# Kernel optimization log

Hardware: AMD Instinct MI355X
Metric: run time of the kernel (lower is better)

The kernel has to match this reference:

```python
import jax, jax.numpy as jnp
import numpy as np

N = 50000      # nodes
DEG = 16       # fixed out-degree per row
E = N * DEG    # edges (CSR nnz)
H = 128        # hidden_size
NH = 8         # num_heads


def setup_inputs() -> dict:
    key = jax.random.key(0)
    ks = jax.random.split(key, 8)
    s = 1.0 / np.sqrt(H)
    h = jax.random.normal(ks[0], (N, H), jnp.float32)
    Wq = jax.random.normal(ks[1], (H, H), jnp.float32) * s
    bq = jax.random.normal(ks[2], (H,), jnp.float32) * 0.02
    Wk = jax.random.normal(ks[3], (H, H), jnp.float32) * s
    bk = jax.random.normal(ks[4], (H,), jnp.float32) * 0.02
    Wv = jax.random.normal(ks[5], (H, H), jnp.float32) * s
    bv = jax.random.normal(ks[6], (H,), jnp.float32) * 0.02
    row_ptr = jnp.arange(N + 1, dtype=jnp.int32) * DEG            # fixed-degree CSR
    col_ind = jax.random.randint(ks[7], (E,), 0, N, dtype=jnp.int32)
    return {"h": h, "Wq": Wq, "bq": bq, "Wk": Wk, "bk": bk, "Wv": Wv, "bv": bv,
            "row_ptr": row_ptr, "col_ind": col_ind, "num_heads": NH}


def reference(h, Wq, bq, Wk, bk, Wv, bv, row_ptr, col_ind, num_heads):
    n = h.shape[0]
    hidden = h.shape[1]
    head_dim = hidden // num_heads
    scaling = head_dim ** (-0.5)
    e = col_ind.shape[0]
    # CSR nnz -> row index per edge
    row = (jnp.searchsorted(row_ptr, jnp.arange(e, dtype=row_ptr.dtype), side="right") - 1).astype(jnp.int32)

    # projections; reshape to (N, head_dim, num_heads) exactly as in the torch code
    q = ((h @ Wq.T + bq) * scaling).reshape(n, head_dim, num_heads)
    k = (h @ Wk.T + bk).reshape(n, head_dim, num_heads)
    v = (h @ Wv.T + bv).reshape(n, head_dim, num_heads)

    # bsddmm: per-edge, per-head dot product over head_dim
    scores = jnp.einsum("edh,edh->eh", q[row], k[col_ind])      # [E, NH]

    # sparse row-wise softmax (segment softmax over edges of each row)
    m = jax.ops.segment_max(scores, row, num_segments=n)        # [N, NH]
    ex = jnp.exp(scores - m[row])
    denom = jax.ops.segment_sum(ex, row, num_segments=n)        # [N, NH]
    attn = ex / denom[row]                                      # [E, NH]

    # bspmm: out[i] = sum_{j in nbr(i)} attn[ij] * v[j]
    out = jax.ops.segment_sum(attn[:, None, :] * v[col_ind], row, num_segments=n)  # [N, head_dim, NH]
    return out.reshape(n, -1)
```

## Files before the change

### kernel.cpp

```cpp
#include <hip/hip_runtime.h>
#include <hip/hip_bf16.h>


typedef unsigned short ushort_t;
typedef unsigned int uint32;
typedef short short8 __attribute__((ext_vector_type(8)));
typedef short short4v __attribute__((ext_vector_type(4)));
typedef float f32x4 __attribute__((ext_vector_type(4)));

#define HID 128
#define DEG 16
#define OSTRIDE_LDS 132

__device__ __forceinline__ float bf2f(ushort_t u) {
  uint32 x = ((uint32)u) << 16;
  return __builtin_bit_cast(float, x);
}
__device__ __forceinline__ ushort_t f2bf(float f) {
  uint32 u = __builtin_bit_cast(uint32, f);
  u += 0x7fffu + ((u >> 16) & 1u);
  return (ushort_t)(u >> 16);
}

__device__ __forceinline__ void split2(float x, float y, uint32& hi, uint32& lo) {
  __hip_bfloat162 h2 = __float22bfloat162_rn(float2{x, y});
  __builtin_memcpy(&hi, &h2, 4);
  float hx = __builtin_bit_cast(float, hi << 16);
  float hy = __builtin_bit_cast(float, hi & 0xffff0000u);
  __hip_bfloat162 l2 = __float22bfloat162_rn(float2{x - hx, y - hy});
  __builtin_memcpy(&lo, &l2, 4);
}

__device__ __forceinline__ void split8v(float4 a, float4 b, short8& hi, short8& lo) {
  uint32* hu = (uint32*)&hi;
  uint32* lu = (uint32*)&lo;
  split2(a.x, a.y, hu[0], lu[0]);
  split2(a.z, a.w, hu[1], lu[1]);
  split2(b.x, b.y, hu[2], lu[2]);
  split2(b.z, b.w, hu[3], lu[3]);
}

__device__ __forceinline__ void split8p(const float* __restrict__ p, short8& hi, short8& lo) {
  float4 a = *(const float4*)p;
  float4 b = *(const float4*)(p + 4);
  split8v(a, b, hi, lo);
}

__global__ __launch_bounds__(256) void prep_kernel(
    const float* __restrict__ Wq, const float* __restrict__ Wk,
    const float* __restrict__ Wv,
    ushort_t* __restrict__ whi, ushort_t* __restrict__ wlo) {
  const int idx8 = (blockIdx.x * 256 + threadIdx.x) * 8;
  const float* W = (idx8 < 16384) ? Wq : (idx8 < 32768) ? Wk : Wv;
  const int off = idx8 & 16383;
  short8 hi, lo;
  split8p(W + off, hi, lo);
  *(short8*)(whi + idx8) = hi;
  *(short8*)(wlo + idx8) = lo;
}

__global__ __launch_bounds__(256) void qkv_fused_kernel(
    const float* __restrict__ h,
    const float* __restrict__ bq, const float* __restrict__ bk,
    const float* __restrict__ bv,
    const ushort_t* __restrict__ whi, const ushort_t* __restrict__ wlo,
    ushort_t* __restrict__ qs, ushort_t* __restrict__ ks, ushort_t* __restrict__ vs,
    int n) {
  __shared__ __align__(16) char lds_b[32 * 1024];
  __shared__ ushort_t lds_r[4][32 * OSTRIDE_LDS];

  const int wave = threadIdx.x >> 6;
  const int l = threadIdx.x & 63;
  const int lm = l & 15;
  const int lq = l >> 4;
  const int m0 = blockIdx.x * 128 + wave * 32;

  int ar0 = m0 + lm;        if (ar0 >= n) ar0 = n - 1;
  int ar1 = m0 + 16 + lm;   if (ar1 >= n) ar1 = n - 1;
  const float* ap0 = h + (size_t)ar0 * HID + lq * 8;
  const float* ap1 = h + (size_t)ar1 * HID + lq * 8;
  short8 ah0[4], al0[4], ah1[4], al1[4];
#pragma unroll
  for (int kt = 0; kt < 4; kt++) {
    split8p(ap0 + kt * 32, ah0[kt], al0[kt]);
    split8p(ap1 + kt * 32, ah1[kt], al1[kt]);
  }

#pragma unroll 1
  for (int p = 0; p < 3; p++) {
    const ushort_t* __restrict__ Wh = whi + p * 16384;
    const ushort_t* __restrict__ Wl = wlo + p * 16384;
    const float* __restrict__ bias = (p == 0) ? bq : (p == 1) ? bk : bv;
    ushort_t* __restrict__ outp = (p == 0) ? qs : (p == 1) ? ks : vs;
    const int ostride = (p == 0) ? 256 : 128;
    const float scale = (p == 0) ? 0.25f : 1.0f;

    f32x4 acc[2][8];
#pragma unroll
    for (int f = 0; f < 2; f++)
#pragma unroll
      for (int t = 0; t < 8; t++) acc[f][t] = (f32x4){0.f, 0.f, 0.f, 0.f};

#pragma unroll
    for (int jj = 0; jj < 8; jj++) {
      const int j = wave * 8 + jj, t = j >> 2, kt = j & 3;
      const ushort_t* gp = Wh + (t * 16 + lm) * HID + kt * 32 + lq * 8;
      __builtin_amdgcn_global_load_lds(
          (const __attribute__((address_space(1))) void*)gp,
          (__attribute__((address_space(3))) void*)(lds_b + j * 1024 + l * 16),
          16, 0, 0);
    }
    __syncthreads();
#pragma unroll
    for (int kt = 0; kt < 4; kt++) {
#pragma unroll
      for (int t = 0; t < 8; t++) {
        short8 bh = *(const short8*)(lds_b + (t * 4 + kt) * 1024 + l * 16);
        acc[0][t] = __builtin_amdgcn_mfma_f32_16x16x32_bf16(ah0[kt], bh, acc[0][t], 0, 0, 0);
        acc[0][t] = __builtin_amdgcn_mfma_f32_16x16x32_bf16(al0[kt], bh, acc[0][t], 0, 0, 0);
        acc[1][t] = __builtin_amdgcn_mfma_f32_16x16x32_bf16(ah1[kt], bh, acc[1][t], 0, 0, 0);
        acc[1][t] = __builtin_amdgcn_mfma_f32_16x16x32_bf16(al1[kt], bh, acc[1][t], 0, 0, 0);
      }
    }
    __syncthreads();

#pragma unroll
    for (int jj = 0; jj < 8; jj++) {
      const int j = wave * 8 + jj, t = j >> 2, kt = j & 3;
      const ushort_t* gp = Wl + (t * 16 + lm) * HID + kt * 32 + lq * 8;
      __builtin_amdgcn_global_load_lds(
          (const __attribute__((address_space(1))) void*)gp,
          (__attribute__((address_space(3))) void*)(lds_b + j * 1024 + l * 16),
          16, 0, 0);
    }
    __syncthreads();
#pragma unroll
    for (int kt = 0; kt < 4; kt++) {
#pragma unroll
      for (int t = 0; t < 8; t++) {
        short8 bl = *(const short8*)(lds_b + (t * 4 + kt) * 1024 + l * 16);
        acc[0][t] = __builtin_amdgcn_mfma_f32_16x16x32_bf16(ah0[kt], bl, acc[0][t], 0, 0, 0);
        acc[1][t] = __builtin_amdgcn_mfma_f32_16x16x32_bf16(ah1[kt], bl, acc[1][t], 0, 0, 0);
      }
    }
    __syncthreads();

    ushort_t* lo_ = lds_r[wave];
#pragma unroll
    for (int t = 0; t < 8; t++) {
      const int col = t * 16 + lm;
      const float bv_ = bias[col];
#pragma unroll
      for (int f = 0; f < 2; f++) {
#pragma unroll
        for (int r = 0; r < 4; r++) {
          lo_[(f * 16 + lq * 4 + r) * OSTRIDE_LDS + col] = f2bf((acc[f][t][r] + bv_) * scale);
        }
      }
    }
    asm volatile("s_waitcnt lgkmcnt(0)" ::: "memory");
    __builtin_amdgcn_wave_barrier();

    const int rr = l >> 5;
    const int ch = l & 31;
#pragma unroll
    for (int it = 0; it < 16; it++) {
      const int rw = it * 2 + rr;
      const int grow = m0 + rw;
      short4v val = *(short4v*)(lo_ + rw * OSTRIDE_LDS + ch * 4);
      if (grow < n) *(short4v*)(outp + (size_t)grow * ostride + ch * 4) = val;
    }
  }
}

__global__ __launch_bounds__(256) void attn_kernel(
    const int* __restrict__ col_ind,
    const ushort_t* __restrict__ qs, const ushort_t* __restrict__ ks,
    const ushort_t* __restrict__ vs, float* __restrict__ out, int n) {
  __shared__ __align__(16) float lds_attn[4 * DEG * 8];

  const int wv = threadIdx.x >> 6;
  const int l = threadIdx.x & 63;
  const int lm = l & 15;
  const int lq = l >> 4;

  int row = blockIdx.x * 4 + wv;
  if (row >= n) row = n - 1;
  const int eb = row * DEG;

  const int cm = col_ind[eb + lm];
  const ushort_t* kp = ks + (size_t)cm * HID + lq * 8;
  const ushort_t* qp = qs + (size_t)row * 256;

  short8 af[4];
  ushort_t qv[4];
#pragma unroll
  for (int kt = 0; kt < 4; kt++) {
    af[kt] = *(const short8*)(kp + kt * 32);
    qv[kt] = (lm < 8) ? qp[kt * 32 + lq * 8 + lm] : (ushort_t)0;
  }

  uint32 vreg[DEG];
#pragma unroll
  for (int e = 0; e < DEG; e++) {
    const int c = col_ind[eb + e];
    vreg[e] = *(const uint32*)(vs + (size_t)c * HID + 2 * l);
  }

  f32x4 acc = (f32x4){0.f, 0.f, 0.f, 0.f};
#pragma unroll
  for (int kt = 0; kt < 4; kt++) {
    short8 bf;
#pragma unroll
    for (int j = 0; j < 8; j++) bf[j] = (lm == j) ? (short)qv[kt] : (short)0;
    acc = __builtin_amdgcn_mfma_f32_16x16x32_bf16(af[kt], bf, acc, 0, 0, 0);
  }

  float m = fmaxf(fmaxf(acc[0], acc[1]), fmaxf(acc[2], acc[3]));
  m = fmaxf(m, __shfl_xor(m, 16, 64));
  m = fmaxf(m, __shfl_xor(m, 32, 64));
  float e0 = __expf(acc[0] - m), e1 = __expf(acc[1] - m);
  float e2 = __expf(acc[2] - m), e3 = __expf(acc[3] - m);
  float s = e0 + e1 + e2 + e3;
  s += __shfl_xor(s, 16, 64);
  s += __shfl_xor(s, 32, 64);
  const float inv = 1.0f / s;

  float* ap = &lds_attn[wv * (DEG * 8)];
  if (lm < 8) {
    ap[(lq * 4 + 0) * 8 + lm] = e0 * inv;
    ap[(lq * 4 + 1) * 8 + lm] = e1 * inv;
    ap[(lq * 4 + 2) * 8 + lm] = e2 * inv;
    ap[(lq * 4 + 3) * 8 + lm] = e3 * inv;
  }
  asm volatile("s_waitcnt lgkmcnt(0)" ::: "memory");
  __builtin_amdgcn_wave_barrier();

  const int h0 = 2 * (l & 3);
  float o0 = 0.f, o1 = 0.f;
#pragma unroll
  for (int e = 0; e < DEG; e++) {
    const float2 at = *(const float2*)(ap + e * 8 + h0);
    o0 += at.x * bf2f((ushort_t)(vreg[e] & 0xffffu));
    o1 += at.y * bf2f((ushort_t)(vreg[e] >> 16));
  }

  float2 o = {o0, o1};
  *(float2*)(out + (size_t)row * HID + 2 * l) = o;
}

extern "C" void kernel_launch(void* const* d_in, const int* in_sizes, int n_in,
                              void* d_out, int out_size, void* d_ws, size_t ws_size,
                              hipStream_t stream) {
  const float* h  = (const float*)d_in[0];
  const float* Wq = (const float*)d_in[1];
  const float* bq = (const float*)d_in[2];
  const float* Wk = (const float*)d_in[3];
  const float* bk = (const float*)d_in[4];
  const float* Wv = (const float*)d_in[5];
  const float* bv = (const float*)d_in[6];
  const int* col_ind = (const int*)d_in[8];

  const int n = in_sizes[0] / HID;

  ushort_t* ks  = (ushort_t*)d_ws;
  ushort_t* vs  = ks + (size_t)n * HID;
  ushort_t* whi = vs + (size_t)n * HID;
  ushort_t* wlo = whi + 3 * 16384;
  ushort_t* qs  = (ushort_t*)d_out;
  float* outf   = (float*)d_out;

  prep_kernel<<<24, 256, 0, stream>>>(Wq, Wk, Wv, whi, wlo);
  qkv_fused_kernel<<<(n + 127) / 128, 256, 0, stream>>>(h, bq, bk, bv, whi, wlo, qs, ks, vs, n);
  attn_kernel<<<(n + 3) / 4, 256, 0, stream>>>(col_ind, qs, ks, vs, outf, n);
}
```

Measured before the change: 173.3 us.

## Double-buffer QKV weight staging and process two rows per wave in attention

The QKV projection kernel now uses two LDS weight buffers. It prefetches the next hi/lo weight slab with global_load_lds and waits on a partial vmcnt instead of fully serialising each load before its MFMA pass. The attention kernel now handles two CSR rows per wave, issuing twice as many independent K/V gathers to raise memory-level parallelism. The cost is more LDS in the projection kernel, which may reduce blocks per CU, and higher register pressure in the attention kernel.

```diff
diff --git a/kernel.cpp b/kernel.cpp
--- a/kernel.cpp
+++ b/kernel.cpp
@@ -59,6 +59,91 @@
   *(short8*)(wlo + idx8) = lo;
 }
 
+#define WAITV(n) asm volatile("s_waitcnt vmcnt(" #n ")" ::: "memory")
+#define BARRIER() __builtin_amdgcn_s_barrier()
+#define MEMPIN() asm volatile("" ::: "memory")
+
+__device__ __forceinline__ void stage_w(const ushort_t* __restrict__ W,
+                                        char* lb, int wave, int l) {
+  const int lm = l & 15, lq = l >> 4;
+#pragma unroll
+  for (int jj = 0; jj < 8; jj++) {
+    const int j = wave * 8 + jj, t = j >> 2, kt = j & 3;
+    const ushort_t* gp = W + (t * 16 + lm) * HID + kt * 32 + lq * 8;
+    __builtin_amdgcn_global_load_lds(
+        (const __attribute__((address_space(1))) void*)gp,
+        (__attribute__((address_space(3))) void*)(lb + j * 1024 + l * 16),
+        16, 0, 0);
+  }
+}
+
+__device__ __forceinline__ void mfma_hi(const char* lb, int l,
+    const short8 ah0[4], const short8 al0[4],
+    const short8 ah1[4], const short8 al1[4], f32x4 acc[2][8]) {
+#pragma unroll
+  for (int kt = 0; kt < 4; kt++) {
+#pragma unroll
+    for (int t = 0; t < 8; t++) {
+      short8 bh = *(const short8*)(lb + (t * 4 + kt) * 1024 + l * 16);
+      acc[0][t] = __builtin_amdgcn_mfma_f32_16x16x32_bf16(ah0[kt], bh, acc[0][t], 0, 0, 0);
+      acc[0][t] = __builtin_amdgcn_mfma_f32_16x16x32_bf16(al0[kt], bh, acc[0][t], 0, 0, 0);
+      acc[1][t] = __builtin_amdgcn_mfma_f32_16x16x32_bf16(ah1[kt], bh, acc[1][t], 0, 0, 0);
+      acc[1][t] = __builtin_amdgcn_mfma_f32_16x16x32_bf16(al1[kt], bh, acc[1][t], 0, 0, 0);
+    }
+  }
+}
+
+__device__ __forceinline__ void mfma_lo(const char* lb, int l,
+    const short8 ah0[4], const short8 ah1[4], f32x4 acc[2][8]) {
+#pragma unroll
+  for (int kt = 0; kt < 4; kt++) {
+#pragma unroll
+    for (int t = 0; t < 8; t++) {
+      short8 bl = *(const short8*)(lb + (t * 4 + kt) * 1024 + l * 16);
+      acc[0][t] = __builtin_amdgcn_mfma_f32_16x16x32_bf16(ah0[kt], bl, acc[0][t], 0, 0, 0);
+      acc[1][t] = __builtin_amdgcn_mfma_f32_16x16x32_bf16(ah1[kt], bl, acc[1][t], 0, 0, 0);
+    }
+  }
+}
+
+__device__ __forceinline__ void zero_acc(f32x4 acc[2][8]) {
+#pragma unroll
+  for (int f = 0; f < 2; f++)
+#pragma unroll
+    for (int t = 0; t < 8; t++) acc[f][t] = (f32x4){0.f, 0.f, 0.f, 0.f};
+}
+
+__device__ __forceinline__ void epilogue(f32x4 acc[2][8],
+    const float* __restrict__ bias, ushort_t* __restrict__ outp,
+    int ostride, float scale, ushort_t* lo_, int m0, int n, int l) {
+  const int lm = l & 15, lq = l >> 4;
+#pragma unroll
+  for (int t = 0; t < 8; t++) {
+    const int col = t * 16 + lm;
+    const float bv_ = bias[col];
+#pragma unroll
+    for (int f = 0; f < 2; f++) {
+#pragma unroll
+      for (int r = 0; r < 4; r++) {
+        lo_[(f * 16 + lq * 4 + r) * OSTRIDE_LDS + col] = f2bf((acc[f][t][r] + bv_) * scale);
+      }
+    }
+  }
+  asm volatile("s_waitcnt lgkmcnt(0)" ::: "memory");
+  __builtin_amdgcn_wave_barrier();
+
+  const int rr = l >> 5;
+  const int ch = l & 31;
+#pragma unroll
+  for (int it = 0; it < 16; it++) {
+    const int rw = it * 2 + rr;
+    const int grow = m0 + rw;
+    short4v val = *(short4v*)(lo_ + rw * OSTRIDE_LDS + ch * 4);
+    if (grow < n) *(short4v*)(outp + (size_t)grow * ostride + ch * 4) = val;
+  }
+  MEMPIN();
+}
+
 __global__ __launch_bounds__(256) void qkv_fused_kernel(
     const float* __restrict__ h,
     const float* __restrict__ bq, const float* __restrict__ bk,
@@ -66,7 +151,7 @@
     const ushort_t* __restrict__ whi, const ushort_t* __restrict__ wlo,
     ushort_t* __restrict__ qs, ushort_t* __restrict__ ks, ushort_t* __restrict__ vs,
     int n) {
-  __shared__ __align__(16) char lds_b[32 * 1024];
+  __shared__ __align__(16) char lds_b[2][32 * 1024];
   __shared__ ushort_t lds_r[4][32 * OSTRIDE_LDS];
 
   const int wave = threadIdx.x >> 6;
@@ -75,6 +160,8 @@
   const int lq = l >> 4;
   const int m0 = blockIdx.x * 128 + wave * 32;
 
+  stage_w(whi, lds_b[0], wave, l);
+
   int ar0 = m0 + lm;        if (ar0 >= n) ar0 = n - 1;
   int ar1 = m0 + 16 + lm;   if (ar1 >= n) ar1 = n - 1;
   const float* ap0 = h + (size_t)ar0 * HID + lq * 8;
@@ -86,167 +173,146 @@
     split8p(ap1 + kt * 32, ah1[kt], al1[kt]);
   }
 
-#pragma unroll 1
-  for (int p = 0; p < 3; p++) {
-    const ushort_t* __restrict__ Wh = whi + p * 16384;
-    const ushort_t* __restrict__ Wl = wlo + p * 16384;
-    const float* __restrict__ bias = (p == 0) ? bq : (p == 1) ? bk : bv;
-    ushort_t* __restrict__ outp = (p == 0) ? qs : (p == 1) ? ks : vs;
-    const int ostride = (p == 0) ? 256 : 128;
-    const float scale = (p == 0) ? 0.25f : 1.0f;
-
-    f32x4 acc[2][8];
-#pragma unroll
-    for (int f = 0; f < 2; f++)
-#pragma unroll
-      for (int t = 0; t < 8; t++) acc[f][t] = (f32x4){0.f, 0.f, 0.f, 0.f};
-
-#pragma unroll
-    for (int jj = 0; jj < 8; jj++) {
-      const int j = wave * 8 + jj, t = j >> 2, kt = j & 3;
-      const ushort_t* gp = Wh + (t * 16 + lm) * HID + kt * 32 + lq * 8;
-      __builtin_amdgcn_global_load_lds(
-          (const __attribute__((address_space(1))) void*)gp,
-          (__attribute__((address_space(3))) void*)(lds_b + j * 1024 + l * 16),
-          16, 0, 0);
-    }
-    __syncthreads();
-#pragma unroll
-    for (int kt = 0; kt < 4; kt++) {
-#pragma unroll
-      for (int t = 0; t < 8; t++) {
-        short8 bh = *(const short8*)(lds_b + (t * 4 + kt) * 1024 + l * 16);
-        acc[0][t] = __builtin_amdgcn_mfma_f32_16x16x32_bf16(ah0[kt], bh, acc[0][t], 0, 0, 0);
-        acc[0][t] = __builtin_amdgcn_mfma_f32_16x16x32_bf16(al0[kt], bh, acc[0][t], 0, 0, 0);
-        acc[1][t] = __builtin_amdgcn_mfma_f32_16x16x32_bf16(ah1[kt], bh, acc[1][t], 0, 0, 0);
-        acc[1][t] = __builtin_amdgcn_mfma_f32_16x16x32_bf16(al1[kt], bh, acc[1][t], 0, 0, 0);
-      }
-    }
-    __syncthreads();
-
-#pragma unroll
-    for (int jj = 0; jj < 8; jj++) {
-      const int j = wave * 8 + jj, t = j >> 2, kt = j & 3;
-      const ushort_t* gp = Wl + (t * 16 + lm) * HID + kt * 32 + lq * 8;
-      __builtin_amdgcn_global_load_lds(
-          (const __attribute__((address_space(1))) void*)gp,
-          (__attribute__((address_space(3))) void*)(lds_b + j * 1024 + l * 16),
-          16, 0, 0);
-    }
-    __syncthreads();
-#pragma unroll
-    for (int kt = 0; kt < 4; kt++) {
-#pragma unroll
-      for (int t = 0; t < 8; t++) {
-        short8 bl = *(const short8*)(lds_b + (t * 4 + kt) * 1024 + l * 16);
-        acc[0][t] = __builtin_amdgcn_mfma_f32_16x16x32_bf16(ah0[kt], bl, acc[0][t], 0, 0, 0);
-        acc[1][t] = __builtin_amdgcn_mfma_f32_16x16x32_bf16(ah1[kt], bl, acc[1][t], 0, 0, 0);
-      }
-    }
-    __syncthreads();
-
-    ushort_t* lo_ = lds_r[wave];
-#pragma unroll
-    for (int t = 0; t < 8; t++) {
-      const int col = t * 16 + lm;
-      const float bv_ = bias[col];
-#pragma unroll
-      for (int f = 0; f < 2; f++) {
-#pragma unroll
-        for (int r = 0; r < 4; r++) {
-          lo_[(f * 16 + lq * 4 + r) * OSTRIDE_LDS + col] = f2bf((acc[f][t][r] + bv_) * scale);
-        }
-      }
-    }
-    asm volatile("s_waitcnt lgkmcnt(0)" ::: "memory");
-    __builtin_amdgcn_wave_barrier();
-
-    const int rr = l >> 5;
-    const int ch = l & 31;
-#pragma unroll
-    for (int it = 0; it < 16; it++) {
-      const int rw = it * 2 + rr;
-      const int grow = m0 + rw;
-      short4v val = *(short4v*)(lo_ + rw * OSTRIDE_LDS + ch * 4);
-      if (grow < n) *(short4v*)(outp + (size_t)grow * ostride + ch * 4) = val;
-    }
-  }
+  f32x4 acc[2][8];
+  ushort_t* lo_ = lds_r[wave];
+
+  stage_w(wlo, lds_b[1], wave, l);
+  WAITV(8); BARRIER();
+  zero_acc(acc);
+  mfma_hi(lds_b[0], l, ah0, al0, ah1, al1, acc);
+  BARRIER();
+  stage_w(whi + 16384, lds_b[0], wave, l);
+  WAITV(8); BARRIER();
+  mfma_lo(lds_b[1], l, ah0, ah1, acc);
+  epilogue(acc, bq, qs, 256, 0.25f, lo_, m0, n, l);
+  BARRIER();
+  stage_w(wlo + 16384, lds_b[1], wave, l);
+  WAITV(8); BARRIER();
+  zero_acc(acc);
+  mfma_hi(lds_b[0], l, ah0, al0, ah1, al1, acc);
+  BARRIER();
+  stage_w(whi + 32768, lds_b[0], wave, l);
+  WAITV(8); BARRIER();
+  mfma_lo(lds_b[1], l, ah0, ah1, acc);
+  epilogue(acc, bk, ks, 128, 1.0f, lo_, m0, n, l);
+  BARRIER();
+  stage_w(wlo + 32768, lds_b[1], wave, l);
+  WAITV(8); BARRIER();
+  zero_acc(acc);
+  mfma_hi(lds_b[0], l, ah0, al0, ah1, al1, acc);
+  BARRIER();
+  WAITV(0); BARRIER();
+  mfma_lo(lds_b[1], l, ah0, ah1, acc);
+  epilogue(acc, bv, vs, 128, 1.0f, lo_, m0, n, l);
 }
 
 __global__ __launch_bounds__(256) void attn_kernel(
     const int* __restrict__ col_ind,
     const ushort_t* __restrict__ qs, const ushort_t* __restrict__ ks,
     const ushort_t* __restrict__ vs, float* __restrict__ out, int n) {
-  __shared__ __align__(16) float lds_attn[4 * DEG * 8];
+  __shared__ __align__(16) float lds_attn[4][2][DEG * 8];
 
   const int wv = threadIdx.x >> 6;
   const int l = threadIdx.x & 63;
   const int lm = l & 15;
   const int lq = l >> 4;
 
-  int row = blockIdx.x * 4 + wv;
-  if (row >= n) row = n - 1;
-  const int eb = row * DEG;
-
-  const int cm = col_ind[eb + lm];
-  const ushort_t* kp = ks + (size_t)cm * HID + lq * 8;
-  const ushort_t* qp = qs + (size_t)row * 256;
-
-  short8 af[4];
-  ushort_t qv[4];
-#pragma unroll
-  for (int kt = 0; kt < 4; kt++) {
-    af[kt] = *(const short8*)(kp + kt * 32);
-    qv[kt] = (lm < 8) ? qp[kt * 32 + lq * 8 + lm] : (ushort_t)0;
-  }
-
-  uint32 vreg[DEG];
+  int row0 = (blockIdx.x * 4 + wv) * 2;
+  if (row0 >= n) row0 = n - 1;
+  int row1 = row0 + 1;
+  if (row1 >= n) row1 = n - 1;
+  const int eb0 = row0 * DEG, eb1 = row1 * DEG;
+
+  const int cm0 = col_ind[eb0 + lm];
+  const int cm1 = col_ind[eb1 + lm];
+  const ushort_t* kp0 = ks + (size_t)cm0 * HID + lq * 8;
+  const ushort_t* kp1 = ks + (size_t)cm1 * HID + lq * 8;
+  const ushort_t* qp0 = qs + (size_t)row0 * 256;
+  const ushort_t* qp1 = qs + (size_t)row1 * 256;
+
+  short8 af0[4], af1[4];
+  ushort_t qv0[4], qv1[4];
+#pragma unroll
+  for (int kt = 0; kt < 4; kt++) {
+    af0[kt] = *(const short8*)(kp0 + kt * 32);
+    af1[kt] = *(const short8*)(kp1 + kt * 32);
+    qv0[kt] = (lm < 8) ? qp0[kt * 32 + lq * 8 + lm] : (ushort_t)0;
+    qv1[kt] = (lm < 8) ? qp1[kt * 32 + lq * 8 + lm] : (ushort_t)0;
+  }
+
+  uint32 vreg0[DEG], vreg1[DEG];
 #pragma unroll
   for (int e = 0; e < DEG; e++) {
-    const int c = col_ind[eb + e];
-    vreg[e] = *(const uint32*)(vs + (size_t)c * HID + 2 * l);
-  }
-
-  f32x4 acc = (f32x4){0.f, 0.f, 0.f, 0.f};
-#pragma unroll
-  for (int kt = 0; kt < 4; kt++) {
-    short8 bf;
-#pragma unroll
-    for (int j = 0; j < 8; j++) bf[j] = (lm == j) ? (short)qv[kt] : (short)0;
-    acc = __builtin_amdgcn_mfma_f32_16x16x32_bf16(af[kt], bf, acc, 0, 0, 0);
-  }
-
-  float m = fmaxf(fmaxf(acc[0], acc[1]), fmaxf(acc[2], acc[3]));
-  m = fmaxf(m, __shfl_xor(m, 16, 64));
-  m = fmaxf(m, __shfl_xor(m, 32, 64));
-  float e0 = __expf(acc[0] - m), e1 = __expf(acc[1] - m);
-  float e2 = __expf(acc[2] - m), e3 = __expf(acc[3] - m);
-  float s = e0 + e1 + e2 + e3;
-  s += __shfl_xor(s, 16, 64);
-  s += __shfl_xor(s, 32, 64);
-  const float inv = 1.0f / s;
-
-  float* ap = &lds_attn[wv * (DEG * 8)];
+    const int c0 = col_ind[eb0 + e];
+    const int c1 = col_ind[eb1 + e];
+    vreg0[e] = *(const uint32*)(vs + (size_t)c0 * HID + 2 * l);
+    vreg1[e] = *(const uint32*)(vs + (size_t)c1 * HID + 2 * l);
+  }
+
+  f32x4 acc0 = (f32x4){0.f, 0.f, 0.f, 0.f};
+  f32x4 acc1 = (f32x4){0.f, 0.f, 0.f, 0.f};
+#pragma unroll
+  for (int kt = 0; kt < 4; kt++) {
+    short8 bf0, bf1;
+#pragma unroll
+    for (int j = 0; j < 8; j++) {
+      bf0[j] = (lm == j) ? (short)qv0[kt] : (short)0;
+      bf1[j] = (lm == j) ? (short)qv1[kt] : (short)0;
+    }
+    acc0 = __builtin_amdgcn_mfma_f32_16x16x32_bf16(af0[kt], bf0, acc0, 0, 0, 0);
+    acc1 = __builtin_amdgcn_mfma_f32_16x16x32_bf16(af1[kt], bf1, acc1, 0, 0, 0);
+  }
+
+  float m0 = fmaxf(fmaxf(acc0[0], acc0[1]), fmaxf(acc0[2], acc0[3]));
+  m0 = fmaxf(m0, __shfl_xor(m0, 16, 64));
+  m0 = fmaxf(m0, __shfl_xor(m0, 32, 64));
+  float e00 = __expf(acc0[0] - m0), e01 = __expf(acc0[1] - m0);
+  float e02 = __expf(acc0[2] - m0), e03 = __expf(acc0[3] - m0);
+  float s0 = e00 + e01 + e02 + e03;
+  s0 += __shfl_xor(s0, 16, 64);
+  s0 += __shfl_xor(s0, 32, 64);
+  const float inv0 = 1.0f / s0;
+  float m1 = fmaxf(fmaxf(acc1[0], acc1[1]), fmaxf(acc1[2], acc1[3]));
+  m1 = fmaxf(m1, __shfl_xor(m1, 16, 64));
+  m1 = fmaxf(m1, __shfl_xor(m1, 32, 64));
+  float e10 = __expf(acc1[0] - m1), e11 = __expf(acc1[1] - m1);
+  float e12 = __expf(acc1[2] - m1), e13 = __expf(acc1[3] - m1);
+  float s1 = e10 + e11 + e12 + e13;
+  s1 += __shfl_xor(s1, 16, 64);
+  s1 += __shfl_xor(s1, 32, 64);
+  const float inv1 = 1.0f / s1;
+
+  float* ap0 = lds_attn[wv][0];
+  float* ap1 = lds_attn[wv][1];
   if (lm < 8) {
-    ap[(lq * 4 + 0) * 8 + lm] = e0 * inv;
-    ap[(lq * 4 + 1) * 8 + lm] = e1 * inv;
-    ap[(lq * 4 + 2) * 8 + lm] = e2 * inv;
-    ap[(lq * 4 + 3) * 8 + lm] = e3 * inv;
+    ap0[(lq * 4 + 0) * 8 + lm] = e00 * inv0;
+    ap0[(lq * 4 + 1) * 8 + lm] = e01 * inv0;
+    ap0[(lq * 4 + 2) * 8 + lm] = e02 * inv0;
+    ap0[(lq * 4 + 3) * 8 + lm] = e03 * inv0;
+    ap1[(lq * 4 + 0) * 8 + lm] = e10 * inv1;
+    ap1[(lq * 4 + 1) * 8 + lm] = e11 * inv1;
+    ap1[(lq * 4 + 2) * 8 + lm] = e12 * inv1;
+    ap1[(lq * 4 + 3) * 8 + lm] = e13 * inv1;
   }
   asm volatile("s_waitcnt lgkmcnt(0)" ::: "memory");
   __builtin_amdgcn_wave_barrier();
 
   const int h0 = 2 * (l & 3);
-  float o0 = 0.f, o1 = 0.f;
+  float o00 = 0.f, o01 = 0.f, o10 = 0.f, o11 = 0.f;
 #pragma unroll
   for (int e = 0; e < DEG; e++) {
-    const float2 at = *(const float2*)(ap + e * 8 + h0);
-    o0 += at.x * bf2f((ushort_t)(vreg[e] & 0xffffu));
-    o1 += at.y * bf2f((ushort_t)(vreg[e] >> 16));
-  }
-
-  float2 o = {o0, o1};
-  *(float2*)(out + (size_t)row * HID + 2 * l) = o;
+    const float2 a0 = *(const float2*)(ap0 + e * 8 + h0);
+    const float2 a1 = *(const float2*)(ap1 + e * 8 + h0);
+    o00 += a0.x * bf2f((ushort_t)(vreg0[e] & 0xffffu));
+    o01 += a0.y * bf2f((ushort_t)(vreg0[e] >> 16));
+    o10 += a1.x * bf2f((ushort_t)(vreg1[e] & 0xffffu));
+    o11 += a1.y * bf2f((ushort_t)(vreg1[e] >> 16));
+  }
+
+  float2 oa = {o00, o01};
+  float2 ob = {o10, o11};
+  *(float2*)(out + (size_t)row0 * HID + 2 * l) = oa;
+  *(float2*)(out + (size_t)row1 * HID + 2 * l) = ob;
 }
 
 extern "C" void kernel_launch(void* const* d_in, const int* in_sizes, int n_in,
@@ -270,7 +336,8 @@
   ushort_t* qs  = (ushort_t*)d_out;
   float* outf   = (float*)d_out;
 
+  const int npairs = (n + 1) / 2;
   prep_kernel<<<24, 256, 0, stream>>>(Wq, Wk, Wv, whi, wlo);
   qkv_fused_kernel<<<(n + 127) / 128, 256, 0, stream>>>(h, bq, bk, bv, whi, wlo, qs, ks, vs, n);
-  attn_kernel<<<(n + 3) / 4, 256, 0, stream>>>(col_ind, qs, ks, vs, outf, n);
-}
+  attn_kernel<<<(npairs + 3) / 4, 256, 0, stream>>>(col_ind, qs, ks, vs, outf, n);
+}
```

Result: slower. 192.0 us (+10.8%).

## Double-buffer weight staging in QKV kernel to overlap loads with MFMA

Applied to the files above, without the earlier changes.

Splits each 32 KB weight tile load into two 16 KB halves held in a double-buffered LDS region, and fully unrolls the Q/K/V passes into a software pipeline. The next half-tile is issued with global_load_lds while MFMAs consume the current one, with vmcnt waits and barriers replacing the full syncthreads pairs. Input rows are loaded as raw float4 before weight staging, so the bf16 split overlaps the first loads. The cost is fragile hand-placed waitcnt logic and more straight-line code.

```diff
diff --git a/kernel.cpp b/kernel.cpp
--- a/kernel.cpp
+++ b/kernel.cpp
@@ -59,6 +59,94 @@
   *(short8*)(wlo + idx8) = lo;
 }
 
+#define WAITV(n) asm volatile("s_waitcnt vmcnt(" #n ")" ::: "memory")
+#define BARRIER() __builtin_amdgcn_s_barrier()
+#define MEMPIN() asm volatile("" ::: "memory")
+
+__device__ __forceinline__ void stage_half(const ushort_t* __restrict__ W,
+                                           char* lb, int half, int wave, int l) {
+  const int lm = l & 15, lq = l >> 4;
+#pragma unroll
+  for (int jj = 0; jj < 4; jj++) {
+    const int j = half * 16 + wave * 4 + jj;
+    const int t = j >> 2, kt = j & 3;
+    const ushort_t* gp = W + (t * 16 + lm) * HID + kt * 32 + lq * 8;
+    __builtin_amdgcn_global_load_lds(
+        (const __attribute__((address_space(1))) void*)gp,
+        (__attribute__((address_space(3))) void*)(lb + (j & 15) * 1024 + l * 16),
+        16, 0, 0);
+  }
+}
+
+__device__ __forceinline__ void mfma_half_hi(const char* lb, int tbase, int l,
+    const short8 ah0[4], const short8 al0[4],
+    const short8 ah1[4], const short8 al1[4], f32x4 acc[2][8]) {
+#pragma unroll
+  for (int kt = 0; kt < 4; kt++) {
+#pragma unroll
+    for (int tt = 0; tt < 4; tt++) {
+      const int t = tbase + tt;
+      short8 bh = *(const short8*)(lb + (tt * 4 + kt) * 1024 + l * 16);
+      acc[0][t] = __builtin_amdgcn_mfma_f32_16x16x32_bf16(ah0[kt], bh, acc[0][t], 0, 0, 0);
+      acc[0][t] = __builtin_amdgcn_mfma_f32_16x16x32_bf16(al0[kt], bh, acc[0][t], 0, 0, 0);
+      acc[1][t] = __builtin_amdgcn_mfma_f32_16x16x32_bf16(ah1[kt], bh, acc[1][t], 0, 0, 0);
+      acc[1][t] = __builtin_amdgcn_mfma_f32_16x16x32_bf16(al1[kt], bh, acc[1][t], 0, 0, 0);
+    }
+  }
+}
+
+__device__ __forceinline__ void mfma_half_lo(const char* lb, int tbase, int l,
+    const short8 ah0[4], const short8 ah1[4], f32x4 acc[2][8]) {
+#pragma unroll
+  for (int kt = 0; kt < 4; kt++) {
+#pragma unroll
+    for (int tt = 0; tt < 4; tt++) {
+      const int t = tbase + tt;
+      short8 bl = *(const short8*)(lb + (tt * 4 + kt) * 1024 + l * 16);
+      acc[0][t] = __builtin_amdgcn_mfma_f32_16x16x32_bf16(ah0[kt], bl, acc[0][t], 0, 0, 0);
+      acc[1][t] = __builtin_amdgcn_mfma_f32_16x16x32_bf16(ah1[kt], bl, acc[1][t], 0, 0, 0);
+    }
+  }
+}
+
+__device__ __forceinline__ void zero_acc(f32x4 acc[2][8]) {
+#pragma unroll
+  for (int f = 0; f < 2; f++)
+#pragma unroll
+    for (int t = 0; t < 8; t++) acc[f][t] = (f32x4){0.f, 0.f, 0.f, 0.f};
+}
+
+__device__ __forceinline__ void epilogue(f32x4 acc[2][8],
+    const float* __restrict__ bias, ushort_t* __restrict__ outp,
+    int ostride, float scale, ushort_t* lo_, int m0, int n, int l) {
+  const int lm = l & 15, lq = l >> 4;
+#pragma unroll
+  for (int t = 0; t < 8; t++) {
+    const int col = t * 16 + lm;
+    const float bv_ = bias[col];
+#pragma unroll
+    for (int f = 0; f < 2; f++) {
+#pragma unroll
+      for (int r = 0; r < 4; r++) {
+        lo_[(f * 16 + lq * 4 + r) * OSTRIDE_LDS + col] = f2bf((acc[f][t][r] + bv_) * scale);
+      }
+    }
+  }
+  asm volatile("s_waitcnt lgkmcnt(0)" ::: "memory");
+  __builtin_amdgcn_wave_barrier();
+
+  const int rr = l >> 5;
+  const int ch = l & 31;
+#pragma unroll
+  for (int it = 0; it < 16; it++) {
+    const int rw = it * 2 + rr;
+    const int grow = m0 + rw;
+    short4v val = *(short4v*)(lo_ + rw * OSTRIDE_LDS + ch * 4);
+    if (grow < n) *(short4v*)(outp + (size_t)grow * ostride + ch * 4) = val;
+  }
+  MEMPIN();
+}
+
 __global__ __launch_bounds__(256) void qkv_fused_kernel(
     const float* __restrict__ h,
     const float* __restrict__ bq, const float* __restrict__ bk,
@@ -66,7 +154,7 @@
     const ushort_t* __restrict__ whi, const ushort_t* __restrict__ wlo,
     ushort_t* __restrict__ qs, ushort_t* __restrict__ ks, ushort_t* __restrict__ vs,
     int n) {
-  __shared__ __align__(16) char lds_b[32 * 1024];
+  __shared__ __align__(16) char lds_b[2][16 * 1024];
   __shared__ ushort_t lds_r[4][32 * OSTRIDE_LDS];
 
   const int wave = threadIdx.x >> 6;
@@ -79,98 +167,79 @@
   int ar1 = m0 + 16 + lm;   if (ar1 >= n) ar1 = n - 1;
   const float* ap0 = h + (size_t)ar0 * HID + lq * 8;
   const float* ap1 = h + (size_t)ar1 * HID + lq * 8;
+  float4 a0[4][2], a1[4][2];
+#pragma unroll
+  for (int kt = 0; kt < 4; kt++) {
+    a0[kt][0] = *(const float4*)(ap0 + kt * 32);
+    a0[kt][1] = *(const float4*)(ap0 + kt * 32 + 4);
+    a1[kt][0] = *(const float4*)(ap1 + kt * 32);
+    a1[kt][1] = *(const float4*)(ap1 + kt * 32 + 4);
+  }
+
+  stage_half(whi, lds_b[0], 0, wave, l);
+  stage_half(whi, lds_b[1], 1, wave, l);
+
   short8 ah0[4], al0[4], ah1[4], al1[4];
 #pragma unroll
   for (int kt = 0; kt < 4; kt++) {
-    split8p(ap0 + kt * 32, ah0[kt], al0[kt]);
-    split8p(ap1 + kt * 32, ah1[kt], al1[kt]);
-  }
-
-#pragma unroll 1
-  for (int p = 0; p < 3; p++) {
-    const ushort_t* __restrict__ Wh = whi + p * 16384;
-    const ushort_t* __restrict__ Wl = wlo + p * 16384;
-    const float* __restrict__ bias = (p == 0) ? bq : (p == 1) ? bk : bv;
-    ushort_t* __restrict__ outp = (p == 0) ? qs : (p == 1) ? ks : vs;
-    const int ostride = (p == 0) ? 256 : 128;
-    const float scale = (p == 0) ? 0.25f : 1.0f;
-
-    f32x4 acc[2][8];
-#pragma unroll
-    for (int f = 0; f < 2; f++)
-#pragma unroll
-      for (int t = 0; t < 8; t++) acc[f][t] = (f32x4){0.f, 0.f, 0.f, 0.f};
-
-#pragma unroll
-    for (int jj = 0; jj < 8; jj++) {
-      const int j = wave * 8 + jj, t = j >> 2, kt = j & 3;
-      const ushort_t* gp = Wh + (t * 16 + lm) * HID + kt * 32 + lq * 8;
-      __builtin_amdgcn_global_load_lds(
-          (const __attribute__((address_space(1))) void*)gp,
-          (__attribute__((address_space(3))) void*)(lds_b + j * 1024 + l * 16),
-          16, 0, 0);
-    }
-    __syncthreads();
-#pragma unroll
-    for (int kt = 0; kt < 4; kt++) {
-#pragma unroll
-      for (int t = 0; t < 8; t++) {
-        short8 bh = *(const short8*)(lds_b + (t * 4 + kt) * 1024 + l * 16);
-        acc[0][t] = __builtin_amdgcn_mfma_f32_16x16x32_bf16(ah0[kt], bh, acc[0][t], 0, 0, 0);
-        acc[0][t] = __builtin_amdgcn_mfma_f32_16x16x32_bf16(al0[kt], bh, acc[0][t], 0, 0, 0);
-        acc[1][t] = __builtin_amdgcn_mfma_f32_16x16x32_bf16(ah1[kt], bh, acc[1][t], 0, 0, 0);
-        acc[1][t] = __builtin_amdgcn_mfma_f32_16x16x32_bf16(al1[kt], bh, acc[1][t], 0, 0, 0);
-      }
-    }
-    __syncthreads();
-
-#pragma unroll
-    for (int jj = 0; jj < 8; jj++) {
-      const int j = wave * 8 + jj, t = j >> 2, kt = j & 3;
-      const ushort_t* gp = Wl + (t * 16 + lm) * HID + kt * 32 + lq * 8;
-      __builtin_amdgcn_global_load_lds(
-          (const __attribute__((address_space(1))) void*)gp,
-          (__attribute__((address_space(3))) void*)(lds_b + j * 1024 + l * 16),
-          16, 0, 0);
-    }
-    __syncthreads();
-#pragma unroll
-    for (int kt = 0; kt < 4; kt++) {
-#pragma unroll
-      for (int t = 0; t < 8; t++) {
-        short8 bl = *(const short8*)(lds_b + (t * 4 + kt) * 1024 + l * 16);
-        acc[0][t] = __builtin_amdgcn_mfma_f32_16x16x32_bf16(ah0[kt], bl, acc[0][t], 0, 0, 0);
-        acc[1][t] = __builtin_amdgcn_mfma_f32_16x16x32_bf16(ah1[kt], bl, acc[1][t], 0, 0, 0);
-      }
-    }
-    __syncthreads();
-
-    ushort_t* lo_ = lds_r[wave];
-#pragma unroll
-    for (int t = 0; t < 8; t++) {
-      const int col = t * 16 + lm;
-      const float bv_ = bias[col];
-#pragma unroll
-      for (int f = 0; f < 2; f++) {
-#pragma unroll
-        for (int r = 0; r < 4; r++) {
-          lo_[(f * 16 + lq * 4 + r) * OSTRIDE_LDS + col] = f2bf((acc[f][t][r] + bv_) * scale);
-        }
-      }
-    }
-    asm volatile("s_waitcnt lgkmcnt(0)" ::: "memory");
-    __builtin_amdgcn_wave_barrier();
-
-    const int rr = l >> 5;
-    const int ch = l & 31;
-#pragma unroll
-    for (int it = 0; it < 16; it++) {
-      const int rw = it * 2 + rr;
-      const int grow = m0 + rw;
-      short4v val = *(short4v*)(lo_ + rw * OSTRIDE_LDS + ch * 4);
-      if (grow < n) *(short4v*)(outp + (size_t)grow * ostride + ch * 4) = val;
-    }
-  }
+    split8v(a0[kt][0], a0[kt][1], ah0[kt], al0[kt]);
+    split8v(a1[kt][0], a1[kt][1], ah1[kt], al1[kt]);
+  }
+
+  f32x4 acc[2][8];
+  ushort_t* lo_ = lds_r[wave];
+
+  WAITV(4); BARRIER();
+  zero_acc(acc);
+  mfma_half_hi(lds_b[0], 0, l, ah0, al0, ah1, al1, acc);
+  BARRIER();
+  stage_half(wlo, lds_b[0], 0, wave, l);
+  WAITV(4); BARRIER();
+  mfma_half_hi(lds_b[1], 4, l, ah0, al0, ah1, al1, acc);
+  BARRIER();
+  stage_half(wlo, lds_b[1], 1, wave, l);
+  WAITV(4); BARRIER();
+  mfma_half_lo(lds_b[0], 0, l, ah0, ah1, acc);
+  BARRIER();
+  stage_half(whi + 16384, lds_b[0], 0, wave, l);
+  WAITV(4); BARRIER();
+  mfma_half_lo(lds_b[1], 4, l, ah0, ah1, acc);
+  epilogue(acc, bq, qs, 256, 0.25f, lo_, m0, n, l);
+  BARRIER();
+  stage_half(whi + 16384, lds_b[1], 1, wave, l);
+  WAITV(4); BARRIER();
+  zero_acc(acc);
+  mfma_half_hi(lds_b[0], 0, l, ah0, al0, ah1, al1, acc);
+  BARRIER();
+  stage_half(wlo + 16384, lds_b[0], 0, wave, l);
+  WAITV(4); BARRIER();
+  mfma_half_hi(lds_b[1], 4, l, ah0, al0, ah1, al1, acc);
+  BARRIER();
+  stage_half(wlo + 16384, lds_b[1], 1, wave, l);
+  WAITV(4); BARRIER();
+  mfma_half_lo(lds_b[0], 0, l, ah0, ah1, acc);
+  BARRIER();
+  stage_half(whi + 32768, lds_b[0], 0, wave, l);
+  WAITV(4); BARRIER();
+  mfma_half_lo(lds_b[1], 4, l, ah0, ah1, acc);
+  epilogue(acc, bk, ks, 128, 1.0f, lo_, m0, n, l);
+  BARRIER();
+  stage_half(whi + 32768, lds_b[1], 1, wave, l);
+  WAITV(4); BARRIER();
+  zero_acc(acc);
+  mfma_half_hi(lds_b[0], 0, l, ah0, al0, ah1, al1, acc);
+  BARRIER();
+  stage_half(wlo + 32768, lds_b[0], 0, wave, l);
+  WAITV(4); BARRIER();
+  mfma_half_hi(lds_b[1], 4, l, ah0, al0, ah1, al1, acc);
+  BARRIER();
+  stage_half(wlo + 32768, lds_b[1], 1, wave, l);
+  WAITV(4); BARRIER();
+  mfma_half_lo(lds_b[0], 0, l, ah0, ah1, acc);
+  BARRIER();
+  WAITV(0); BARRIER();
+  mfma_half_lo(lds_b[1], 4, l, ah0, ah1, acc);
+  epilogue(acc, bv, vs, 128, 1.0f, lo_, m0, n, l);
 }
 
 __global__ __launch_bounds__(256) void attn_kernel(
```

Measured after the change: 185.2 us. 1.07x slower.
